# Performance work log

Hardware: AMD Instinct MI355X
Metric: run time of the kernel (lower is better)

The kernel has to match this reference:

```python
import jax, jax.numpy as jnp
import numpy as np

N_NODES = 100000
N_EDGES = 640000
EMB = 128
BATCH = 16384
N_REL = 2
HIDDEN = [128, 64, 32]
LN_EPS = 1e-5
NORM_EPS = 1e-12


def setup_inputs() -> dict:
    key = jax.random.key(0)
    ks = jax.random.split(key, 24)
    inp = {}
    inp["user_indices"] = jax.random.randint(ks[0], (BATCH,), 0, N_NODES)
    inp["item_indices"] = jax.random.randint(ks[1], (BATCH,), 0, N_NODES)
    inp["edge_index"] = jax.random.randint(ks[2], (2, N_EDGES), 0, N_NODES)
    inp["edge_type"] = jax.random.randint(ks[3], (N_EDGES,), 0, N_REL)
    inp["edge_weight"] = jax.random.uniform(ks[4], (N_EDGES,), dtype=jnp.float32)
    # parameters
    s = 1.0 / np.sqrt(EMB)
    inp["embedding"] = jax.random.normal(ks[5], (N_NODES, EMB), jnp.float32) * 0.02
    inp["w1_rel"] = jax.random.normal(ks[6], (N_REL, EMB, EMB), jnp.float32) * s
    inp["w1_root"] = jax.random.normal(ks[7], (EMB, EMB), jnp.float32) * s
    inp["b1"] = jnp.zeros((EMB,), jnp.float32)
    inp["ln_g"] = jnp.ones((EMB,), jnp.float32)
    inp["ln_b"] = jnp.zeros((EMB,), jnp.float32)
    inp["w2_rel"] = jax.random.normal(ks[8], (N_REL, EMB, EMB), jnp.float32) * s
    inp["w2_root"] = jax.random.normal(ks[9], (EMB, EMB), jnp.float32) * s
    inp["b2"] = jnp.zeros((EMB,), jnp.float32)
    dims = [2 * EMB] + HIDDEN
    for i in range(len(HIDDEN)):
        inp[f"mlp_w{i}"] = jax.random.normal(ks[10 + i], (dims[i], dims[i + 1]), jnp.float32) / np.sqrt(dims[i])
        inp[f"mlp_b{i}"] = jnp.zeros((dims[i + 1],), jnp.float32)
    d_out = HIDDEN[-1] + EMB
    inp["out_w"] = jax.random.normal(ks[20], (d_out, 1), jnp.float32) / np.sqrt(d_out)
    inp["out_b"] = jnp.zeros((1,), jnp.float32)
    return inp


def rgcn_layer(x, edge_index, edge_type, edge_weight, w_rel, w_root, bias):
    # x: [N, D]; edge_index: [2, E]; per-relation linear on gathered source feats,
    # weighted scatter-add into destination nodes, plus root transform + bias.
    src, dst = edge_index[0], edge_index[1]
    x_j = x[src]  # [E, D] gather
    msg = jnp.zeros((x_j.shape[0], w_rel.shape[2]), x.dtype)
    for r in range(w_rel.shape[0]):  # small fixed relation count
        msg = msg + jnp.where((edge_type == r)[:, None], x_j @ w_rel[r], 0.0)
    msg = msg * edge_weight[:, None]
    agg = jax.ops.segment_sum(msg, dst, num_segments=x.shape[0])
    return agg + x @ w_root + bias


def layer_norm(x, g, b):
    mu = jnp.mean(x, axis=-1, keepdims=True)
    var = jnp.mean(jnp.square(x - mu), axis=-1, keepdims=True)
    return (x - mu) * jax.lax.rsqrt(var + LN_EPS) * g + b


def l2_normalize(x):
    n = jnp.sqrt(jnp.sum(jnp.square(x), axis=-1, keepdims=True))
    return x / jnp.maximum(n, NORM_EPS)


def reference(user_indices, item_indices, edge_index, edge_type, edge_weight,
              embedding, w1_rel, w1_root, b1, ln_g, ln_b, w2_rel, w2_root, b2,
              mlp_w0, mlp_b0, mlp_w1, mlp_b1, mlp_w2, mlp_b2, out_w, out_b):
    x = embedding  # embedding(arange(N)) == full table
    x = rgcn_layer(x, edge_index, edge_type, edge_weight, w1_rel, w1_root, b1)
    x = jax.nn.relu(x)
    # dropout is identity in eval mode
    x = layer_norm(x, ln_g, ln_b)
    x = rgcn_layer(x, edge_index, edge_type, edge_weight, w2_rel, w2_root, b2)

    u = x[user_indices]  # [B, D]
    v = x[item_indices]
    gmf = l2_normalize(u) * l2_normalize(v)  # [B, D]
    h = jnp.concatenate([u, v], axis=-1)  # [B, 2D]
    for w, b in ((mlp_w0, mlp_b0), (mlp_w1, mlp_b1), (mlp_w2, mlp_b2)):
        h = jax.nn.relu(h @ w + b)
    final = jnp.concatenate([gmf, h], axis=-1)  # [B, D + 32]
    score = jax.nn.sigmoid(final @ out_w + out_b)
    return jnp.squeeze(score, axis=-1)
```

## Files before the change

kernel.cpp:

```cpp
#include <hip/hip_runtime.h>
#include <cstddef>
#include <cstdint>

#define N_NODES 100000
#define N_EDGES 640000
#define EMBD    128
#define NBATCH  16384
#define CHUNK   1024
#define NCHUNK  ((N_NODES + CHUNK - 1) / CHUNK)

typedef short bf16x8 __attribute__((ext_vector_type(8)));
typedef float f32x4  __attribute__((ext_vector_type(4)));

__device__ __forceinline__ unsigned pack_split(float x) {
    unsigned u  = __float_as_uint(x);
    unsigned hi = (u + 0x7fffu + ((u >> 16) & 1u)) & 0xffff0000u;
    float    lo = x - __uint_as_float(hi);
    unsigned ul = __float_as_uint(lo);
    unsigned lw = ((ul + 0x7fffu + ((ul >> 16) & 1u)) >> 16) & 0xffffu;
    return hi | lw;
}
__device__ __forceinline__ float unpack_split(unsigned u) {
    return __uint_as_float(u & 0xffff0000u) + __uint_as_float(u << 16);
}

__global__ __launch_bounds__(256) void pack_hist(
    const float* __restrict__ emb, unsigned* __restrict__ xslot,
    const int* __restrict__ ei, int* __restrict__ cursor, int n, int E)
{
    const int i = blockIdx.x * 256 + threadIdx.x;
    if (i < n) xslot[i] = pack_split(emb[i]);
    if (i < E) atomicAdd(&cursor[ei[E + i]], 1);
}

__global__ __launch_bounds__(256) void scan_local(
    int* __restrict__ cursor, int* __restrict__ bsum, int n)
{
    __shared__ int part[256];
    const int t    = threadIdx.x;
    const int base = blockIdx.x * CHUNK + t * 4;
    int v[4];
    int s = 0;
#pragma unroll
    for (int i = 0; i < 4; ++i) {
        const int idx = base + i;
        v[i] = (idx < n) ? cursor[idx] : 0;
        s += v[i];
    }
    part[t] = s;
    __syncthreads();
    for (int off = 1; off < 256; off <<= 1) {
        const int add = (t >= off) ? part[t - off] : 0;
        __syncthreads();
        part[t] += add;
        __syncthreads();
    }
    if (t == 255) bsum[blockIdx.x] = part[255];
    int run = (t == 0) ? 0 : part[t - 1];
#pragma unroll
    for (int i = 0; i < 4; ++i) {
        const int idx = base + i;
        if (idx < n) { cursor[idx] = run; run += v[i]; }
    }
}

__global__ __launch_bounds__(128) void scan_bsum(int* __restrict__ bsum)
{
    __shared__ int part[128];
    const int t = threadIdx.x;
    const int v = (t < NCHUNK) ? bsum[t] : 0;
    part[t] = v;
    __syncthreads();
    for (int off = 1; off < 128; off <<= 1) {
        const int add = (t >= off) ? part[t - off] : 0;
        __syncthreads();
        part[t] += add;
        __syncthreads();
    }
    if (t < NCHUNK) bsum[t] = part[t] - v;
}

__global__ __launch_bounds__(256) void scan_add(
    int* __restrict__ cursor, const int* __restrict__ bsum, int n)
{
    const int off  = bsum[blockIdx.x];
    const int base = blockIdx.x * CHUNK + threadIdx.x * 4;
#pragma unroll
    for (int i = 0; i < 4; ++i) {
        const int idx = base + i;
        if (idx < n) cursor[idx] += off;
    }
}

__global__ __launch_bounds__(256) void bucket_kernel(
    const int* __restrict__ ei, const int* __restrict__ et,
    const float* __restrict__ ew, int* __restrict__ cursor,
    int2* __restrict__ srec, int E)
{
    const int e = blockIdx.x * 256 + threadIdx.x;
    if (e >= E) return;
    const int src = ei[e];
    const int dst = ei[E + e];
    const int r   = et[e];
    const int pos = atomicAdd(&cursor[dst], 1);
    srec[pos] = make_int2(src | (r << 17), __float_as_int(ew[e]));
}

__global__ __launch_bounds__(256) void accum_csr(
    const unsigned* __restrict__ xp, const int2* __restrict__ srec,
    const int* __restrict__ cursor, unsigned* __restrict__ Ap, int N)
{
    const int wid  = blockIdx.x * 4 + (threadIdx.x >> 6);
    const int lane = threadIdx.x & 63;
    const int s = (wid == 0) ? 0 : cursor[wid - 1];
    const int e = cursor[wid];

    float ax = 0.f, ay = 0.f, bx = 0.f, by = 0.f;
    int i = s;
    for (; i + 3 < e; i += 4) {
        const int2 r0 = srec[i];
        const int2 r1 = srec[i + 1];
        const int2 r2 = srec[i + 2];
        const int2 r3 = srec[i + 3];
        const uint2 g0 = ((const uint2*)(xp + (size_t)(r0.x & 0x1FFFF) * EMBD))[lane];
        const uint2 g1 = ((const uint2*)(xp + (size_t)(r1.x & 0x1FFFF) * EMBD))[lane];
        const uint2 g2 = ((const uint2*)(xp + (size_t)(r2.x & 0x1FFFF) * EMBD))[lane];
        const uint2 g3 = ((const uint2*)(xp + (size_t)(r3.x & 0x1FFFF) * EMBD))[lane];
        const float w0 = __int_as_float(r0.y);
        const float w1 = __int_as_float(r1.y);
        const float w2 = __int_as_float(r2.y);
        const float w3 = __int_as_float(r3.y);
        {
            const float vx = unpack_split(g0.x), vy = unpack_split(g0.y);
            if (r0.x & (1 << 17)) { bx += vx * w0; by += vy * w0; }
            else                  { ax += vx * w0; ay += vy * w0; }
        }
        {
            const float vx = unpack_split(g1.x), vy = unpack_split(g1.y);
            if (r1.x & (1 << 17)) { bx += vx * w1; by += vy * w1; }
            else                  { ax += vx * w1; ay += vy * w1; }
        }
        {
            const float vx = unpack_split(g2.x), vy = unpack_split(g2.y);
            if (r2.x & (1 << 17)) { bx += vx * w2; by += vy * w2; }
            else                  { ax += vx * w2; ay += vy * w2; }
        }
        {
            const float vx = unpack_split(g3.x), vy = unpack_split(g3.y);
            if (r3.x & (1 << 17)) { bx += vx * w3; by += vy * w3; }
            else                  { ax += vx * w3; ay += vy * w3; }
        }
    }
    for (; i < e; ++i) {
        const int2 r0 = srec[i];
        const uint2 g0 = ((const uint2*)(xp + (size_t)(r0.x & 0x1FFFF) * EMBD))[lane];
        const float w0 = __int_as_float(r0.y);
        const float vx = unpack_split(g0.x), vy = unpack_split(g0.y);
        if (r0.x & (1 << 17)) { bx += vx * w0; by += vy * w0; }
        else                  { ax += vx * w0; ay += vy * w0; }
    }
    ((uint2*)(Ap + (size_t)wid * EMBD))[lane]       = make_uint2(pack_split(ax), pack_split(ay));
    ((uint2*)(Ap + ((size_t)N + wid) * EMBD))[lane] = make_uint2(pack_split(bx), pack_split(by));
}

__global__ __launch_bounds__(256) void gemm_mfma(
    const unsigned* __restrict__ S0, const unsigned* __restrict__ S1,
    const unsigned* __restrict__ S2,
    const float* __restrict__ wrel, const float* __restrict__ wroot,
    const float* __restrict__ bias, const float* __restrict__ lng,
    const float* __restrict__ lnb, void* __restrict__ outv,
    int M, int do_ln)
{
    __shared__ unsigned short AsH[128 * 40], AsL[128 * 40];
    __shared__ unsigned short BsH[128 * 40], BsL[128 * 40];
    __shared__ float lnbuf[2][128][2];

    const int t    = threadIdx.x;
    const int wave = t >> 6;
    const int lane = t & 63;
    const int q    = lane >> 4;
    const int n    = lane & 15;
    const int wrow = wave & 1;
    const int wcol = wave >> 1;
    const int m0   = blockIdx.x * 128;

    const int arow  = t >> 1;
    const int ahalf = t & 1;
    const int bcol  = t & 127;
    const int bkh   = t >> 7;

    f32x4 acc[4][4];
#pragma unroll
    for (int rt = 0; rt < 4; ++rt)
#pragma unroll
        for (int ct = 0; ct < 4; ++ct)
            acc[rt][ct] = (f32x4){0.f, 0.f, 0.f, 0.f};

    uint4 au0, au1, au2, au3;
    auto loadA = [&](int kc) {
        const unsigned* Sp = (kc < 4) ? S0 : (kc < 8) ? S1 : S2;
        const int rg = m0 + arow;
        if (rg < M) {
            const unsigned* p = Sp + (size_t)rg * EMBD + (kc & 3) * 32 + ahalf * 16;
            au0 = *(const uint4*)(p);
            au1 = *(const uint4*)(p + 4);
            au2 = *(const uint4*)(p + 8);
            au3 = *(const uint4*)(p + 12);
        } else {
            au0 = au1 = au2 = au3 = make_uint4(0u, 0u, 0u, 0u);
        }
    };

    loadA(0);

    for (int kc = 0; kc < 12; ++kc) {
        __syncthreads();

        {
            const unsigned uu[16] = {au0.x, au0.y, au0.z, au0.w,
                                     au1.x, au1.y, au1.z, au1.w,
                                     au2.x, au2.y, au2.z, au2.w,
                                     au3.x, au3.y, au3.z, au3.w};
            unsigned dh[8], dl[8];
#pragma unroll
            for (int i = 0; i < 8; ++i) {
                const unsigned e0 = uu[2 * i], e1 = uu[2 * i + 1];
                dh[i] = (e1 & 0xffff0000u) | (e0 >> 16);
                dl[i] = (e1 << 16) | (e0 & 0xffffu);
            }
            uint4* pH = (uint4*)(AsH + arow * 40 + ahalf * 16);
            uint4* pL = (uint4*)(AsL + arow * 40 + ahalf * 16);
            pH[0] = make_uint4(dh[0], dh[1], dh[2], dh[3]);
            pH[1] = make_uint4(dh[4], dh[5], dh[6], dh[7]);
            pL[0] = make_uint4(dl[0], dl[1], dl[2], dl[3]);
            pL[1] = make_uint4(dl[4], dl[5], dl[6], dl[7]);
        }

        if (kc < 11) loadA(kc + 1);

        {
            const float* Wsrc = (kc < 8) ? (wrel + (size_t)kc * 32 * EMBD)
                                         : (wroot + (size_t)(kc - 8) * 32 * EMBD);
            unsigned pk[16];
#pragma unroll
            for (int j = 0; j < 16; ++j)
                pk[j] = pack_split(Wsrc[(size_t)(bkh * 16 + j) * EMBD + bcol]);
            unsigned dh[8], dl[8];
#pragma unroll
            for (int i = 0; i < 8; ++i) {
                const unsigned e0 = pk[2 * i], e1 = pk[2 * i + 1];
                dh[i] = (e1 & 0xffff0000u) | (e0 >> 16);
                dl[i] = (e1 << 16) | (e0 & 0xffffu);
            }
            uint4* pH = (uint4*)(BsH + bcol * 40 + bkh * 16);
            uint4* pL = (uint4*)(BsL + bcol * 40 + bkh * 16);
            pH[0] = make_uint4(dh[0], dh[1], dh[2], dh[3]);
            pH[1] = make_uint4(dh[4], dh[5], dh[6], dh[7]);
            pL[0] = make_uint4(dl[0], dl[1], dl[2], dl[3]);
            pL[1] = make_uint4(dl[4], dl[5], dl[6], dl[7]);
        }
        __syncthreads();

        bf16x8 ah[4], al[4];
#pragma unroll
        for (int rt = 0; rt < 4; ++rt) {
            const int r = wrow * 64 + rt * 16 + n;
            ah[rt] = *(const bf16x8*)&AsH[r * 40 + q * 8];
            al[rt] = *(const bf16x8*)&AsL[r * 40 + q * 8];
        }
#pragma unroll
        for (int ct = 0; ct < 4; ++ct) {
            const int c = wcol * 64 + ct * 16 + n;
            const bf16x8 bh = *(const bf16x8*)&BsH[c * 40 + q * 8];
            const bf16x8 bl = *(const bf16x8*)&BsL[c * 40 + q * 8];
#pragma unroll
            for (int rt = 0; rt < 4; ++rt) {
                acc[rt][ct] = __builtin_amdgcn_mfma_f32_16x16x32_bf16(ah[rt], bh, acc[rt][ct], 0, 0, 0);
                acc[rt][ct] = __builtin_amdgcn_mfma_f32_16x16x32_bf16(ah[rt], bl, acc[rt][ct], 0, 0, 0);
                acc[rt][ct] = __builtin_amdgcn_mfma_f32_16x16x32_bf16(al[rt], bh, acc[rt][ct], 0, 0, 0);
            }
        }
    }

    float bb[4], gg[4], tb[4];
#pragma unroll
    for (int ct = 0; ct < 4; ++ct) {
        const int c = wcol * 64 + ct * 16 + n;
        bb[ct] = bias[c];
        gg[ct] = do_ln ? lng[c] : 0.f;
        tb[ct] = do_ln ? lnb[c] : 0.f;
    }

    if (do_ln) {
#pragma unroll
        for (int rt = 0; rt < 4; ++rt)
#pragma unroll
            for (int r = 0; r < 4; ++r) {
                float s = 0.f, sq = 0.f;
#pragma unroll
                for (int ct = 0; ct < 4; ++ct) {
                    float v = acc[rt][ct][r] + bb[ct];
                    v = fmaxf(v, 0.f);
                    acc[rt][ct][r] = v;
                    s += v; sq += v * v;
                }
#pragma unroll
                for (int off = 1; off < 16; off <<= 1) {
                    s  += __shfl_xor(s,  off, 64);
                    sq += __shfl_xor(sq, off, 64);
                }
                if (n == 0) {
                    const int row = wrow * 64 + rt * 16 + q * 4 + r;
                    lnbuf[wcol][row][0] = s;
                    lnbuf[wcol][row][1] = sq;
                }
            }
        __syncthreads();
        unsigned* outp = (unsigned*)outv;
#pragma unroll
        for (int rt = 0; rt < 4; ++rt)
#pragma unroll
            for (int r = 0; r < 4; ++r) {
                const int row = wrow * 64 + rt * 16 + q * 4 + r;
                const int rg  = m0 + row;
                const float s    = lnbuf[0][row][0] + lnbuf[1][row][0];
                const float sq   = lnbuf[0][row][1] + lnbuf[1][row][1];
                const float mu   = s * (1.0f / 128.0f);
                const float var  = sq * (1.0f / 128.0f) - mu * mu;
                const float rstd = rsqrtf(var + 1e-5f);
                if (rg < M) {
#pragma unroll
                    for (int ct = 0; ct < 4; ++ct) {
                        const int c = wcol * 64 + ct * 16 + n;
                        const float v = (acc[rt][ct][r] - mu) * rstd * gg[ct] + tb[ct];
                        outp[(size_t)rg * EMBD + c] = pack_split(v);
                    }
                }
            }
    } else {
        float* outp = (float*)outv;
#pragma unroll
        for (int rt = 0; rt < 4; ++rt)
#pragma unroll
            for (int r = 0; r < 4; ++r) {
                const int rg = m0 + wrow * 64 + rt * 16 + q * 4 + r;
                if (rg < M) {
#pragma unroll
                    for (int ct = 0; ct < 4; ++ct) {
                        const int c = wcol * 64 + ct * 16 + n;
                        outp[(size_t)rg * EMBD + c] = acc[rt][ct][r] + bb[ct];
                    }
                }
            }
    }
}

__global__ __launch_bounds__(256) void head_kernel(
    const float* __restrict__ x2, const int* __restrict__ ui, const int* __restrict__ vi,
    const float* __restrict__ mw0, const float* __restrict__ mb0,
    const float* __restrict__ mw1, const float* __restrict__ mb1,
    const float* __restrict__ mw2, const float* __restrict__ mb2,
    const float* __restrict__ ow, const float* __restrict__ ob,
    float* __restrict__ out, int B)
{
    __shared__ float h0[16][256];
    __shared__ float h1[16][128];
    __shared__ float h2[16][64];
    __shared__ float h3[16][32];
    __shared__ float ps_u[16][16], ps_v[16][16];
    __shared__ float inv_nunv[16];
    __shared__ float pg[16][16], ph[16][16];

    const int t   = threadIdx.x;
    const int bb0 = blockIdx.x * 16;

    for (int r = 0; r < 16; ++r) {
        const int b   = bb0 + r;
        const int idx = (t < 128) ? ui[b] : vi[b];
        const int c   = t & 127;
        h0[r][t] = x2[(size_t)idx * EMBD + c];
    }
    __syncthreads();

    {
        const int row = t >> 4, sub = t & 15;
        float su = 0.f, sv = 0.f;
#pragma unroll
        for (int k = 0; k < 8; ++k) {
            const float a = h0[row][sub + 16 * k];       su += a * a;
            const float b = h0[row][128 + sub + 16 * k]; sv += b * b;
        }
        ps_u[row][sub] = su; ps_v[row][sub] = sv;
    }
    __syncthreads();
    if (t < 16) {
        float su = 0.f, sv = 0.f;
#pragma unroll
        for (int k = 0; k < 16; ++k) { su += ps_u[t][k]; sv += ps_v[t][k]; }
        const float nu = fmaxf(sqrtf(su), 1e-12f);
        const float nv = fmaxf(sqrtf(sv), 1e-12f);
        inv_nunv[t] = 1.0f / (nu * nv);
    }
    __syncthreads();

    {
        const int c = t & 127, rr = t >> 7;
        float acc[8];
#pragma unroll
        for (int j = 0; j < 8; ++j) acc[j] = 0.f;
        for (int i = 0; i < 256; i += 4) {
            const float w0 = mw0[(i + 0) * 128 + c];
            const float w1 = mw0[(i + 1) * 128 + c];
            const float w2 = mw0[(i + 2) * 128 + c];
            const float w3 = mw0[(i + 3) * 128 + c];
#pragma unroll
            for (int j = 0; j < 8; ++j) {
                const float4 a = *(const float4*)&h0[rr * 8 + j][i];
                acc[j] += a.x * w0 + a.y * w1 + a.z * w2 + a.w * w3;
            }
        }
        const float bv = mb0[c];
#pragma unroll
        for (int j = 0; j < 8; ++j) h1[rr * 8 + j][c] = fmaxf(acc[j] + bv, 0.f);
    }
    __syncthreads();

    {
        const int c = t & 63, g = t >> 6;
        float acc[4] = {0.f, 0.f, 0.f, 0.f};
        for (int i = 0; i < 128; i += 4) {
            const float w0 = mw1[(i + 0) * 64 + c];
            const float w1 = mw1[(i + 1) * 64 + c];
            const float w2 = mw1[(i + 2) * 64 + c];
            const float w3 = mw1[(i + 3) * 64 + c];
#pragma unroll
            for (int j = 0; j < 4; ++j) {
                const float4 a = *(const float4*)&h1[g * 4 + j][i];
                acc[j] += a.x * w0 + a.y * w1 + a.z * w2 + a.w * w3;
            }
        }
        const float bv = mb1[c];
#pragma unroll
        for (int j = 0; j < 4; ++j) h2[g * 4 + j][c] = fmaxf(acc[j] + bv, 0.f);
    }
    __syncthreads();

    {
        const int c = t & 31, g = t >> 5;
        float acc[2] = {0.f, 0.f};
        for (int i = 0; i < 64; i += 4) {
            const float w0 = mw2[(i + 0) * 32 + c];
            const float w1 = mw2[(i + 1) * 32 + c];
            const float w2 = mw2[(i + 2) * 32 + c];
            const float w3 = mw2[(i + 3) * 32 + c];
#pragma unroll
            for (int j = 0; j < 2; ++j) {
                const float4 a = *(const float4*)&h2[g * 2 + j][i];
                acc[j] += a.x * w0 + a.y * w1 + a.z * w2 + a.w * w3;
            }
        }
        const float bv = mb2[c];
#pragma unroll
        for (int j = 0; j < 2; ++j) h3[g * 2 + j][c] = fmaxf(acc[j] + bv, 0.f);
    }
    __syncthreads();

    {
        const int row = t >> 4, sub = t & 15;
        float pgv = 0.f;
#pragma unroll
        for (int k = 0; k < 8; ++k) {
            const int c = sub + 16 * k;
            pgv += h0[row][c] * h0[row][128 + c] * ow[c];
        }
        const float phv = h3[row][sub]      * ow[128 + sub]
                        + h3[row][sub + 16] * ow[144 + sub];
        pg[row][sub] = pgv; ph[row][sub] = phv;
    }
    __syncthreads();
    if (t < 16) {
        float sg = 0.f, sh = 0.f;
#pragma unroll
        for (int k = 0; k < 16; ++k) { sg += pg[t][k]; sh += ph[t][k]; }
        const float z = sg * inv_nunv[t] + sh + ob[0];
        out[bb0 + t] = 1.0f / (1.0f + expf(-z));
    }
}

extern "C" void kernel_launch(void* const* d_in, const int* in_sizes, int n_in,
                              void* d_out, int out_size, void* d_ws, size_t ws_size,
                              hipStream_t stream)
{
    const int*   ui      = (const int*)d_in[0];
    const int*   vi      = (const int*)d_in[1];
    const int*   ei      = (const int*)d_in[2];
    const int*   et      = (const int*)d_in[3];
    const float* ew      = (const float*)d_in[4];
    const float* emb     = (const float*)d_in[5];
    const float* w1_rel  = (const float*)d_in[6];
    const float* w1_root = (const float*)d_in[7];
    const float* b1      = (const float*)d_in[8];
    const float* ln_g    = (const float*)d_in[9];
    const float* ln_b    = (const float*)d_in[10];
    const float* w2_rel  = (const float*)d_in[11];
    const float* w2_root = (const float*)d_in[12];
    const float* b2      = (const float*)d_in[13];
    const float* mw0     = (const float*)d_in[14];
    const float* mb0     = (const float*)d_in[15];
    const float* mw1     = (const float*)d_in[16];
    const float* mb1     = (const float*)d_in[17];
    const float* mw2     = (const float*)d_in[18];
    const float* mb2     = (const float*)d_in[19];
    const float* ow      = (const float*)d_in[20];
    const float* ob      = (const float*)d_in[21];
    float* out = (float*)d_out;

    const int N = N_NODES, E = N_EDGES, B = NBATCH;

    unsigned* Ap    = (unsigned*)d_ws;
    unsigned* xslot = Ap + (size_t)2 * N * EMBD;
    int2*     srec   = (int2*)(xslot + (size_t)N * EMBD);
    int*      cursor = (int*)(srec + E);
    int*      bsum   = cursor + N;

    float* x2 = (float*)Ap;

    hipMemsetAsync(cursor, 0, N * sizeof(int), stream);
    pack_hist<<<(N * EMBD + 255) / 256, 256, 0, stream>>>(emb, xslot, ei, cursor, N * EMBD, E);

    scan_local<<<NCHUNK, 256, 0, stream>>>(cursor, bsum, N);
    scan_bsum<<<1, 128, 0, stream>>>(bsum);
    scan_add<<<NCHUNK, 256, 0, stream>>>(cursor, bsum, N);
    bucket_kernel<<<(E + 255) / 256, 256, 0, stream>>>(ei, et, ew, cursor, srec, E);

    const int ggrid = (N + 127) / 128;

    accum_csr<<<N / 4, 256, 0, stream>>>(xslot, srec, cursor, Ap, N);
    gemm_mfma<<<ggrid, 256, 0, stream>>>(
        Ap, Ap + (size_t)N * EMBD, xslot,
        w1_rel, w1_root, b1, ln_g, ln_b, (void*)xslot, N, 1);

    accum_csr<<<N / 4, 256, 0, stream>>>(xslot, srec, cursor, Ap, N);
    gemm_mfma<<<ggrid, 256, 0, stream>>>(
        Ap, Ap + (size_t)N * EMBD, xslot,
        w2_rel, w2_root, b2, nullptr, nullptr, (void*)x2, N, 0);

    head_kernel<<<B / 16, 256, 0, stream>>>(
        x2, ui, vi, mw0, mb0, mw1, mb1, mw2, mb2, ow, ob, out, B);
}
```

Measured before the change: 499.7 us.

## Split node features into bf16 hi/lo planes and gather only the hi plane

Features are stored as separate bf16 high and low planes instead of interleaved hi/lo words. The edge aggregation now gathers only the high plane and writes its result as plain bf16. This halves the bytes moved by the memory-bound gather and halves the aggregate writes. The GEMM drops the low-part MFMA for the aggregated operand and skips the repacking shuffle. The separate block-sum scan kernel is folded into scan_add, which removes one launch. The cost is lower precision in the message aggregation, since the low-order correction bits of source features and aggregates are discarded.

New measurement: 597.0 us. 19.5% more time.

```diff
diff --git a/kernel.cpp b/kernel.cpp
--- a/kernel.cpp
+++ b/kernel.cpp
@@ -20,16 +20,25 @@
     unsigned lw = ((ul + 0x7fffu + ((ul >> 16) & 1u)) >> 16) & 0xffffu;
     return hi | lw;
 }
-__device__ __forceinline__ float unpack_split(unsigned u) {
-    return __uint_as_float(u & 0xffff0000u) + __uint_as_float(u << 16);
+__device__ __forceinline__ unsigned short f2bf(float x) {
+    unsigned u = __float_as_uint(x);
+    return (unsigned short)((u + 0x7fffu + ((u >> 16) & 1u)) >> 16);
+}
+__device__ __forceinline__ float bf2f(unsigned short h) {
+    return __uint_as_float((unsigned)h << 16);
 }
 
 __global__ __launch_bounds__(256) void pack_hist(
-    const float* __restrict__ emb, unsigned* __restrict__ xslot,
+    const float* __restrict__ emb,
+    unsigned short* __restrict__ xhi, unsigned short* __restrict__ xlo,
     const int* __restrict__ ei, int* __restrict__ cursor, int n, int E)
 {
     const int i = blockIdx.x * 256 + threadIdx.x;
-    if (i < n) xslot[i] = pack_split(emb[i]);
+    if (i < n) {
+        const unsigned p = pack_split(emb[i]);
+        xhi[i] = (unsigned short)(p >> 16);
+        xlo[i] = (unsigned short)(p & 0xffffu);
+    }
     if (i < E) atomicAdd(&cursor[ei[E + i]], 1);
 }
 
@@ -64,31 +73,24 @@
     }
 }
 
-__global__ __launch_bounds__(128) void scan_bsum(int* __restrict__ bsum)
-{
-    __shared__ int part[128];
-    const int t = threadIdx.x;
-    const int v = (t < NCHUNK) ? bsum[t] : 0;
-    part[t] = v;
-    __syncthreads();
-    for (int off = 1; off < 128; off <<= 1) {
-        const int add = (t >= off) ? part[t - off] : 0;
-        __syncthreads();
-        part[t] += add;
-        __syncthreads();
-    }
-    if (t < NCHUNK) bsum[t] = part[t] - v;
-}
-
 __global__ __launch_bounds__(256) void scan_add(
     int* __restrict__ cursor, const int* __restrict__ bsum, int n)
 {
-    const int off  = bsum[blockIdx.x];
-    const int base = blockIdx.x * CHUNK + threadIdx.x * 4;
+    __shared__ int red[256];
+    const int t = threadIdx.x;
+    const int b = blockIdx.x;
+    red[t] = (t < b && t < NCHUNK) ? bsum[t] : 0;
+    __syncthreads();
+    for (int off = 128; off > 0; off >>= 1) {
+        if (t < off) red[t] += red[t + off];
+        __syncthreads();
+    }
+    const int off_ = red[0];
+    const int base = b * CHUNK + t * 4;
 #pragma unroll
     for (int i = 0; i < 4; ++i) {
         const int idx = base + i;
-        if (idx < n) cursor[idx] += off;
+        if (idx < n) cursor[idx] += off_;
     }
 }
 
@@ -107,8 +109,8 @@
 }
 
 __global__ __launch_bounds__(256) void accum_csr(
-    const unsigned* __restrict__ xp, const int2* __restrict__ srec,
-    const int* __restrict__ cursor, unsigned* __restrict__ Ap, int N)
+    const unsigned short* __restrict__ xhi, const int2* __restrict__ srec,
+    const int* __restrict__ cursor, unsigned short* __restrict__ Ahi, int N)
 {
     const int wid  = blockIdx.x * 4 + (threadIdx.x >> 6);
     const int lane = threadIdx.x & 63;
@@ -122,54 +124,63 @@
         const int2 r1 = srec[i + 1];
         const int2 r2 = srec[i + 2];
         const int2 r3 = srec[i + 3];
-        const uint2 g0 = ((const uint2*)(xp + (size_t)(r0.x & 0x1FFFF) * EMBD))[lane];
-        const uint2 g1 = ((const uint2*)(xp + (size_t)(r1.x & 0x1FFFF) * EMBD))[lane];
-        const uint2 g2 = ((const uint2*)(xp + (size_t)(r2.x & 0x1FFFF) * EMBD))[lane];
-        const uint2 g3 = ((const uint2*)(xp + (size_t)(r3.x & 0x1FFFF) * EMBD))[lane];
+        const unsigned g0 = ((const unsigned*)(xhi + (size_t)(r0.x & 0x1FFFF) * EMBD))[lane];
+        const unsigned g1 = ((const unsigned*)(xhi + (size_t)(r1.x & 0x1FFFF) * EMBD))[lane];
+        const unsigned g2 = ((const unsigned*)(xhi + (size_t)(r2.x & 0x1FFFF) * EMBD))[lane];
+        const unsigned g3 = ((const unsigned*)(xhi + (size_t)(r3.x & 0x1FFFF) * EMBD))[lane];
         const float w0 = __int_as_float(r0.y);
         const float w1 = __int_as_float(r1.y);
         const float w2 = __int_as_float(r2.y);
         const float w3 = __int_as_float(r3.y);
         {
-            const float vx = unpack_split(g0.x), vy = unpack_split(g0.y);
+            const float vx = bf2f((unsigned short)(g0 & 0xffffu));
+            const float vy = bf2f((unsigned short)(g0 >> 16));
             if (r0.x & (1 << 17)) { bx += vx * w0; by += vy * w0; }
             else                  { ax += vx * w0; ay += vy * w0; }
         }
         {
-            const float vx = unpack_split(g1.x), vy = unpack_split(g1.y);
+            const float vx = bf2f((unsigned short)(g1 & 0xffffu));
+            const float vy = bf2f((unsigned short)(g1 >> 16));
             if (r1.x & (1 << 17)) { bx += vx * w1; by += vy * w1; }
             else                  { ax += vx * w1; ay += vy * w1; }
         }
         {
-            const float vx = unpack_split(g2.x), vy = unpack_split(g2.y);
+            const float vx = bf2f((unsigned short)(g2 & 0xffffu));
+            const float vy = bf2f((unsigned short)(g2 >> 16));
             if (r2.x & (1 << 17)) { bx += vx * w2; by += vy * w2; }
             else                  { ax += vx * w2; ay += vy * w2; }
         }
         {
-            const float vx = unpack_split(g3.x), vy = unpack_split(g3.y);
+            const float vx = bf2f((unsigned short)(g3 & 0xffffu));
+            const float vy = bf2f((unsigned short)(g3 >> 16));
             if (r3.x & (1 << 17)) { bx += vx * w3; by += vy * w3; }
             else                  { ax += vx * w3; ay += vy * w3; }
         }
     }
     for (; i < e; ++i) {
         const int2 r0 = srec[i];
-        const uint2 g0 = ((const uint2*)(xp + (size_t)(r0.x & 0x1FFFF) * EMBD))[lane];
+        const unsigned g0 = ((const unsigned*)(xhi + (size_t)(r0.x & 0x1FFFF) * EMBD))[lane];
         const float w0 = __int_as_float(r0.y);
-        const float vx = unpack_split(g0.x), vy = unpack_split(g0.y);
+        const float vx = bf2f((unsigned short)(g0 & 0xffffu));
+        const float vy = bf2f((unsigned short)(g0 >> 16));
         if (r0.x & (1 << 17)) { bx += vx * w0; by += vy * w0; }
         else                  { ax += vx * w0; ay += vy * w0; }
     }
-    ((uint2*)(Ap + (size_t)wid * EMBD))[lane]       = make_uint2(pack_split(ax), pack_split(ay));
-    ((uint2*)(Ap + ((size_t)N + wid) * EMBD))[lane] = make_uint2(pack_split(bx), pack_split(by));
+    ((unsigned*)(Ahi + (size_t)wid * EMBD))[lane] =
+        (unsigned)f2bf(ax) | ((unsigned)f2bf(ay) << 16);
+    ((unsigned*)(Ahi + ((size_t)N + wid) * EMBD))[lane] =
+        (unsigned)f2bf(bx) | ((unsigned)f2bf(by) << 16);
 }
 
 __global__ __launch_bounds__(256) void gemm_mfma(
-    const unsigned* __restrict__ S0, const unsigned* __restrict__ S1,
-    const unsigned* __restrict__ S2,
+    const unsigned short* __restrict__ Ahi,
+    const unsigned short* __restrict__ xhi, const unsigned short* __restrict__ xlo,
     const float* __restrict__ wrel, const float* __restrict__ wroot,
     const float* __restrict__ bias, const float* __restrict__ lng,
-    const float* __restrict__ lnb, void* __restrict__ outv,
-    int M, int do_ln)
+    const float* __restrict__ lnb,
+    unsigned short* __restrict__ oh, unsigned short* __restrict__ ol,
+    float* __restrict__ of,
+    int M, int N, int do_ln)
 {
     __shared__ unsigned short AsH[128 * 40], AsL[128 * 40];
     __shared__ unsigned short BsH[128 * 40], BsL[128 * 40];
@@ -196,18 +207,24 @@
         for (int ct = 0; ct < 4; ++ct)
             acc[rt][ct] = (f32x4){0.f, 0.f, 0.f, 0.f};
 
-    uint4 au0, au1, au2, au3;
+    uint4 auh0, auh1, aul0, aul1;
     auto loadA = [&](int kc) {
-        const unsigned* Sp = (kc < 4) ? S0 : (kc < 8) ? S1 : S2;
         const int rg = m0 + arow;
         if (rg < M) {
-            const unsigned* p = Sp + (size_t)rg * EMBD + (kc & 3) * 32 + ahalf * 16;
-            au0 = *(const uint4*)(p);
-            au1 = *(const uint4*)(p + 4);
-            au2 = *(const uint4*)(p + 8);
-            au3 = *(const uint4*)(p + 12);
+            if (kc < 8) {
+                const unsigned short* p =
+                    Ahi + ((size_t)((kc >> 2) & 1) * N + rg) * EMBD + (kc & 3) * 32 + ahalf * 16;
+                auh0 = *(const uint4*)(p);
+                auh1 = *(const uint4*)(p + 8);
+            } else {
+                const size_t o = (size_t)rg * EMBD + (kc - 8) * 32 + ahalf * 16;
+                auh0 = *(const uint4*)(xhi + o);
+                auh1 = *(const uint4*)(xhi + o + 8);
+                aul0 = *(const uint4*)(xlo + o);
+                aul1 = *(const uint4*)(xlo + o + 8);
+            }
         } else {
-            au0 = au1 = au2 = au3 = make_uint4(0u, 0u, 0u, 0u);
+            auh0 = auh1 = aul0 = aul1 = make_uint4(0u, 0u, 0u, 0u);
         }
     };
 
@@ -217,23 +234,12 @@
         __syncthreads();
 
         {
-            const unsigned uu[16] = {au0.x, au0.y, au0.z, au0.w,
-                                     au1.x, au1.y, au1.z, au1.w,
-                                     au2.x, au2.y, au2.z, au2.w,
-                                     au3.x, au3.y, au3.z, au3.w};
-            unsigned dh[8], dl[8];
-#pragma unroll
-            for (int i = 0; i < 8; ++i) {
-                const unsigned e0 = uu[2 * i], e1 = uu[2 * i + 1];
-                dh[i] = (e1 & 0xffff0000u) | (e0 >> 16);
-                dl[i] = (e1 << 16) | (e0 & 0xffffu);
-            }
             uint4* pH = (uint4*)(AsH + arow * 40 + ahalf * 16);
-            uint4* pL = (uint4*)(AsL + arow * 40 + ahalf * 16);
-            pH[0] = make_uint4(dh[0], dh[1], dh[2], dh[3]);
-            pH[1] = make_uint4(dh[4], dh[5], dh[6], dh[7]);
-            pL[0] = make_uint4(dl[0], dl[1], dl[2], dl[3]);
-            pL[1] = make_uint4(dl[4], dl[5], dl[6], dl[7]);
+            pH[0] = auh0; pH[1] = auh1;
+            if (kc >= 8) {
+                uint4* pL = (uint4*)(AsL + arow * 40 + ahalf * 16);
+                pL[0] = aul0; pL[1] = aul1;
+            }
         }
 
         if (kc < 11) loadA(kc + 1);
@@ -261,23 +267,42 @@
         }
         __syncthreads();
 
-        bf16x8 ah[4], al[4];
+        bf16x8 ah[4];
 #pragma unroll
         for (int rt = 0; rt < 4; ++rt) {
             const int r = wrow * 64 + rt * 16 + n;
             ah[rt] = *(const bf16x8*)&AsH[r * 40 + q * 8];
-            al[rt] = *(const bf16x8*)&AsL[r * 40 + q * 8];
-        }
-#pragma unroll
-        for (int ct = 0; ct < 4; ++ct) {
-            const int c = wcol * 64 + ct * 16 + n;
-            const bf16x8 bh = *(const bf16x8*)&BsH[c * 40 + q * 8];
-            const bf16x8 bl = *(const bf16x8*)&BsL[c * 40 + q * 8];
+        }
+        if (kc < 8) {
+#pragma unroll
+            for (int ct = 0; ct < 4; ++ct) {
+                const int c = wcol * 64 + ct * 16 + n;
+                const bf16x8 bh = *(const bf16x8*)&BsH[c * 40 + q * 8];
+                const bf16x8 bl = *(const bf16x8*)&BsL[c * 40 + q * 8];
+#pragma unroll
+                for (int rt = 0; rt < 4; ++rt) {
+                    acc[rt][ct] = __builtin_amdgcn_mfma_f32_16x16x32_bf16(ah[rt], bh, acc[rt][ct], 0, 0, 0);
+                    acc[rt][ct] = __builtin_amdgcn_mfma_f32_16x16x32_bf16(ah[rt], bl, acc[rt][ct], 0, 0, 0);
+                }
+            }
+        } else {
+            bf16x8 al[4];
 #pragma unroll
             for (int rt = 0; rt < 4; ++rt) {
-                acc[rt][ct] = __builtin_amdgcn_mfma_f32_16x16x32_bf16(ah[rt], bh, acc[rt][ct], 0, 0, 0);
-                acc[rt][ct] = __builtin_amdgcn_mfma_f32_16x16x32_bf16(ah[rt], bl, acc[rt][ct], 0, 0, 0);
-                acc[rt][ct] = __builtin_amdgcn_mfma_f32_16x16x32_bf16(al[rt], bh, acc[rt][ct], 0, 0, 0);
+                const int r = wrow * 64 + rt * 16 + n;
+                al[rt] = *(const bf16x8*)&AsL[r * 40 + q * 8];
+            }
+#pragma unroll
+            for (int ct = 0; ct < 4; ++ct) {
+                const int c = wcol * 64 + ct * 16 + n;
+                const bf16x8 bh = *(const bf16x8*)&BsH[c * 40 + q * 8];
+                const bf16x8 bl = *(const bf16x8*)&BsL[c * 40 + q * 8];
+#pragma unroll
+                for (int rt = 0; rt < 4; ++rt) {
+                    acc[rt][ct] = __builtin_amdgcn_mfma_f32_16x16x32_bf16(ah[rt], bh, acc[rt][ct], 0, 0, 0);
+                    acc[rt][ct] = __builtin_amdgcn_mfma_f32_16x16x32_bf16(ah[rt], bl, acc[rt][ct], 0, 0, 0);
+                    acc[rt][ct] = __builtin_amdgcn_mfma_f32_16x16x32_bf16(al[rt], bh, acc[rt][ct], 0, 0, 0);
+                }
             }
         }
     }
@@ -316,7 +341,6 @@
                 }
             }
         __syncthreads();
-        unsigned* outp = (unsigned*)outv;
 #pragma unroll
         for (int rt = 0; rt < 4; ++rt)
 #pragma unroll
@@ -333,12 +357,13 @@
                     for (int ct = 0; ct < 4; ++ct) {
                         const int c = wcol * 64 + ct * 16 + n;
                         const float v = (acc[rt][ct][r] - mu) * rstd * gg[ct] + tb[ct];
-                        outp[(size_t)rg * EMBD + c] = pack_split(v);
+                        const unsigned p = pack_split(v);
+                        oh[(size_t)rg * EMBD + c] = (unsigned short)(p >> 16);
+                        ol[(size_t)rg * EMBD + c] = (unsigned short)(p & 0xffffu);
                     }
                 }
             }
     } else {
-        float* outp = (float*)outv;
 #pragma unroll
         for (int rt = 0; rt < 4; ++rt)
 #pragma unroll
@@ -348,7 +373,7 @@
 #pragma unroll
                     for (int ct = 0; ct < 4; ++ct) {
                         const int c = wcol * 64 + ct * 16 + n;
-                        outp[(size_t)rg * EMBD + c] = acc[rt][ct][r] + bb[ct];
+                        of[(size_t)rg * EMBD + c] = acc[rt][ct][r] + bb[ct];
                     }
                 }
             }
@@ -517,33 +542,33 @@
 
     const int N = N_NODES, E = N_EDGES, B = NBATCH;
 
-    unsigned* Ap    = (unsigned*)d_ws;
-    unsigned* xslot = Ap + (size_t)2 * N * EMBD;
-    int2*     srec   = (int2*)(xslot + (size_t)N * EMBD);
-    int*      cursor = (int*)(srec + E);
-    int*      bsum   = cursor + N;
-
-    float* x2 = (float*)Ap;
+    unsigned short* Ahi = (unsigned short*)d_ws;
+    unsigned short* xhi = Ahi + (size_t)2 * N * EMBD;
+    unsigned short* xlo = xhi + (size_t)N * EMBD;
+    float*          x2  = (float*)(xlo + (size_t)N * EMBD);
+    int2*   srec   = (int2*)(x2 + (size_t)N * EMBD);
+    int*    cursor = (int*)(srec + E);
+    int*    bsum   = cursor + N;
 
     hipMemsetAsync(cursor, 0, N * sizeof(int), stream);
-    pack_hist<<<(N * EMBD + 255) / 256, 256, 0, stream>>>(emb, xslot, ei, cursor, N * EMBD, E);
+    pack_hist<<<(N * EMBD + 255) / 256, 256, 0, stream>>>(
+        emb, xhi, xlo, ei, cursor, N * EMBD, E);
 
     scan_local<<<NCHUNK, 256, 0, stream>>>(cursor, bsum, N);
-    scan_bsum<<<1, 128, 0, stream>>>(bsum);
     scan_add<<<NCHUNK, 256, 0, stream>>>(cursor, bsum, N);
     bucket_kernel<<<(E + 255) / 256, 256, 0, stream>>>(ei, et, ew, cursor, srec, E);
 
     const int ggrid = (N + 127) / 128;
 
-    accum_csr<<<N / 4, 256, 0, stream>>>(xslot, srec, cursor, Ap, N);
+    accum_csr<<<N / 4, 256, 0, stream>>>(xhi, srec, cursor, Ahi, N);
     gemm_mfma<<<ggrid, 256, 0, stream>>>(
-        Ap, Ap + (size_t)N * EMBD, xslot,
-        w1_rel, w1_root, b1, ln_g, ln_b, (void*)xslot, N, 1);
-
-    accum_csr<<<N / 4, 256, 0, stream>>>(xslot, srec, cursor, Ap, N);
+        Ahi, xhi, xlo, w1_rel, w1_root, b1, ln_g, ln_b,
+        xhi, xlo, nullptr, N, N, 1);
+
+    accum_csr<<<N / 4, 256, 0, stream>>>(xhi, srec, cursor, Ahi, N);
     gemm_mfma<<<ggrid, 256, 0, stream>>>(
-        Ap, Ap + (size_t)N * EMBD, xslot,
-        w2_rel, w2_root, b2, nullptr, nullptr, (void*)x2, N, 0);
+        Ahi, xhi, xlo, w2_rel, w2_root, b2, nullptr, nullptr,
+        nullptr, nullptr, x2, N, N, 0);
 
     head_kernel<<<B / 16, 256, 0, stream>>>(
         x2, ui, vi, mw0, mb0, mw1, mb1, mw2, mb2, ow, ob, out, B);
```

## Gather bf16-only feature copy in edge aggregation and fold block-sum scan

Applied to the files above, without the earlier changes.

Writes a second, bf16-high-half-only copy of node features (in pack_hist and the LN gemm epilogue) and has the CSR aggregation gather that copy, halving gather bytes per edge. It also removes the single-block scan_bsum kernel by having each scan_add block reduce its prefix of block sums itself, and vectorises pack_hist to two floats per thread. The new path drops the low bf16 correction term, which loses precision in messages, and it needs extra workspace, falling back to the old path when the workspace is too small.

Result: faster. 482.6 us (-3.4%).

```diff
diff --git a/kernel.cpp b/kernel.cpp
--- a/kernel.cpp
+++ b/kernel.cpp
@@ -23,14 +23,24 @@
 __device__ __forceinline__ float unpack_split(unsigned u) {
     return __uint_as_float(u & 0xffff0000u) + __uint_as_float(u << 16);
 }
+__device__ __forceinline__ float bf2f(unsigned short h) {
+    return __uint_as_float((unsigned)h << 16);
+}
 
 __global__ __launch_bounds__(256) void pack_hist(
-    const float* __restrict__ emb, unsigned* __restrict__ xslot,
-    const int* __restrict__ ei, int* __restrict__ cursor, int n, int E)
-{
-    const int i = blockIdx.x * 256 + threadIdx.x;
-    if (i < n) xslot[i] = pack_split(emb[i]);
-    if (i < E) atomicAdd(&cursor[ei[E + i]], 1);
+    const float* __restrict__ emb, unsigned* __restrict__ xp,
+    unsigned short* __restrict__ xh,
+    const int* __restrict__ ei, int* __restrict__ cursor, int n2, int E)
+{
+    const int j = blockIdx.x * 256 + threadIdx.x;
+    if (j < n2) {
+        const float2 v = ((const float2*)emb)[j];
+        const unsigned p0 = pack_split(v.x);
+        const unsigned p1 = pack_split(v.y);
+        ((uint2*)xp)[j] = make_uint2(p0, p1);
+        if (xh) ((unsigned*)xh)[j] = (p0 >> 16) | (p1 & 0xffff0000u);
+    }
+    if (j < E) atomicAdd(&cursor[ei[E + j]], 1);
 }
 
 __global__ __launch_bounds__(256) void scan_local(
@@ -64,31 +74,24 @@
     }
 }
 
-__global__ __launch_bounds__(128) void scan_bsum(int* __restrict__ bsum)
-{
-    __shared__ int part[128];
-    const int t = threadIdx.x;
-    const int v = (t < NCHUNK) ? bsum[t] : 0;
-    part[t] = v;
-    __syncthreads();
-    for (int off = 1; off < 128; off <<= 1) {
-        const int add = (t >= off) ? part[t - off] : 0;
-        __syncthreads();
-        part[t] += add;
-        __syncthreads();
-    }
-    if (t < NCHUNK) bsum[t] = part[t] - v;
-}
-
 __global__ __launch_bounds__(256) void scan_add(
     int* __restrict__ cursor, const int* __restrict__ bsum, int n)
 {
-    const int off  = bsum[blockIdx.x];
-    const int base = blockIdx.x * CHUNK + threadIdx.x * 4;
+    __shared__ int red[256];
+    const int t = threadIdx.x;
+    const int b = blockIdx.x;
+    red[t] = (t < b && t < NCHUNK) ? bsum[t] : 0;
+    __syncthreads();
+    for (int off = 128; off > 0; off >>= 1) {
+        if (t < off) red[t] += red[t + off];
+        __syncthreads();
+    }
+    const int off_ = red[0];
+    const int base = b * CHUNK + t * 4;
 #pragma unroll
     for (int i = 0; i < 4; ++i) {
         const int idx = base + i;
-        if (idx < n) cursor[idx] += off;
+        if (idx < n) cursor[idx] += off_;
     }
 }
 
@@ -106,9 +109,11 @@
     srec[pos] = make_int2(src | (r << 17), __float_as_int(ew[e]));
 }
 
+template <bool HI>
 __global__ __launch_bounds__(256) void accum_csr(
-    const unsigned* __restrict__ xp, const int2* __restrict__ srec,
-    const int* __restrict__ cursor, unsigned* __restrict__ Ap, int N)
+    const unsigned* __restrict__ xp, const unsigned short* __restrict__ xh,
+    const int2* __restrict__ srec, const int* __restrict__ cursor,
+    unsigned* __restrict__ Ap, int N)
 {
     const int wid  = blockIdx.x * 4 + (threadIdx.x >> 6);
     const int lane = threadIdx.x & 63;
@@ -116,48 +121,50 @@
     const int e = cursor[wid];
 
     float ax = 0.f, ay = 0.f, bx = 0.f, by = 0.f;
+
+    auto fetch = [&](int src, float& vx, float& vy) {
+        if (HI) {
+            const unsigned g = ((const unsigned*)(xh + (size_t)src * EMBD))[lane];
+            vx = bf2f((unsigned short)(g & 0xffffu));
+            vy = bf2f((unsigned short)(g >> 16));
+        } else {
+            const uint2 g = ((const uint2*)(xp + (size_t)src * EMBD))[lane];
+            vx = unpack_split(g.x);
+            vy = unpack_split(g.y);
+        }
+    };
+
     int i = s;
     for (; i + 3 < e; i += 4) {
         const int2 r0 = srec[i];
         const int2 r1 = srec[i + 1];
         const int2 r2 = srec[i + 2];
         const int2 r3 = srec[i + 3];
-        const uint2 g0 = ((const uint2*)(xp + (size_t)(r0.x & 0x1FFFF) * EMBD))[lane];
-        const uint2 g1 = ((const uint2*)(xp + (size_t)(r1.x & 0x1FFFF) * EMBD))[lane];
-        const uint2 g2 = ((const uint2*)(xp + (size_t)(r2.x & 0x1FFFF) * EMBD))[lane];
-        const uint2 g3 = ((const uint2*)(xp + (size_t)(r3.x & 0x1FFFF) * EMBD))[lane];
+        float x0, y0, x1, y1, x2v, y2v, x3, y3;
+        fetch(r0.x & 0x1FFFF, x0, y0);
+        fetch(r1.x & 0x1FFFF, x1, y1);
+        fetch(r2.x & 0x1FFFF, x2v, y2v);
+        fetch(r3.x & 0x1FFFF, x3, y3);
         const float w0 = __int_as_float(r0.y);
         const float w1 = __int_as_float(r1.y);
         const float w2 = __int_as_float(r2.y);
         const float w3 = __int_as_float(r3.y);
-        {
-            const float vx = unpack_split(g0.x), vy = unpack_split(g0.y);
-            if (r0.x & (1 << 17)) { bx += vx * w0; by += vy * w0; }
-            else                  { ax += vx * w0; ay += vy * w0; }
-        }
-        {
-            const float vx = unpack_split(g1.x), vy = unpack_split(g1.y);
-            if (r1.x & (1 << 17)) { bx += vx * w1; by += vy * w1; }
-            else                  { ax += vx * w1; ay += vy * w1; }
-        }
-        {
-            const float vx = unpack_split(g2.x), vy = unpack_split(g2.y);
-            if (r2.x & (1 << 17)) { bx += vx * w2; by += vy * w2; }
-            else                  { ax += vx * w2; ay += vy * w2; }
-        }
-        {
-            const float vx = unpack_split(g3.x), vy = unpack_split(g3.y);
-            if (r3.x & (1 << 17)) { bx += vx * w3; by += vy * w3; }
-            else                  { ax += vx * w3; ay += vy * w3; }
-        }
+        if (r0.x & (1 << 17)) { bx += x0 * w0;  by += y0 * w0; }
+        else                  { ax += x0 * w0;  ay += y0 * w0; }
+        if (r1.x & (1 << 17)) { bx += x1 * w1;  by += y1 * w1; }
+        else                  { ax += x1 * w1;  ay += y1 * w1; }
+        if (r2.x & (1 << 17)) { bx += x2v * w2; by += y2v * w2; }
+        else                  { ax += x2v * w2; ay += y2v * w2; }
+        if (r3.x & (1 << 17)) { bx += x3 * w3;  by += y3 * w3; }
+        else                  { ax += x3 * w3;  ay += y3 * w3; }
     }
     for (; i < e; ++i) {
         const int2 r0 = srec[i];
-        const uint2 g0 = ((const uint2*)(xp + (size_t)(r0.x & 0x1FFFF) * EMBD))[lane];
+        float x0, y0;
+        fetch(r0.x & 0x1FFFF, x0, y0);
         const float w0 = __int_as_float(r0.y);
-        const float vx = unpack_split(g0.x), vy = unpack_split(g0.y);
-        if (r0.x & (1 << 17)) { bx += vx * w0; by += vy * w0; }
-        else                  { ax += vx * w0; ay += vy * w0; }
+        if (r0.x & (1 << 17)) { bx += x0 * w0; by += y0 * w0; }
+        else                  { ax += x0 * w0; ay += y0 * w0; }
     }
     ((uint2*)(Ap + (size_t)wid * EMBD))[lane]       = make_uint2(pack_split(ax), pack_split(ay));
     ((uint2*)(Ap + ((size_t)N + wid) * EMBD))[lane] = make_uint2(pack_split(bx), pack_split(by));
@@ -169,6 +176,7 @@
     const float* __restrict__ wrel, const float* __restrict__ wroot,
     const float* __restrict__ bias, const float* __restrict__ lng,
     const float* __restrict__ lnb, void* __restrict__ outv,
+    unsigned short* __restrict__ ohi,
     int M, int do_ln)
 {
     __shared__ unsigned short AsH[128 * 40], AsL[128 * 40];
@@ -333,7 +341,9 @@
                     for (int ct = 0; ct < 4; ++ct) {
                         const int c = wcol * 64 + ct * 16 + n;
                         const float v = (acc[rt][ct][r] - mu) * rstd * gg[ct] + tb[ct];
-                        outp[(size_t)rg * EMBD + c] = pack_split(v);
+                        const unsigned p = pack_split(v);
+                        outp[(size_t)rg * EMBD + c] = p;
+                        if (ohi) ohi[(size_t)rg * EMBD + c] = (unsigned short)(p >> 16);
                     }
                 }
             }
@@ -517,33 +527,40 @@
 
     const int N = N_NODES, E = N_EDGES, B = NBATCH;
 
-    unsigned* Ap    = (unsigned*)d_ws;
-    unsigned* xslot = Ap + (size_t)2 * N * EMBD;
-    int2*     srec   = (int2*)(xslot + (size_t)N * EMBD);
-    int*      cursor = (int*)(srec + E);
-    int*      bsum   = cursor + N;
+    unsigned* Ap = (unsigned*)d_ws;
+    unsigned* xp = Ap + (size_t)2 * N * EMBD;
+    int2*   srec   = (int2*)(xp + (size_t)N * EMBD);
+    int*    cursor = (int*)(srec + E);
+    int*    bsum   = cursor + N;
+    unsigned short* xhi = (unsigned short*)(bsum + NCHUNK);
+
+    const size_t need_hi = (size_t)((char*)(xhi + (size_t)N * EMBD) - (char*)d_ws);
+    const bool have_hi = (ws_size >= need_hi);
+    unsigned short* xh = have_hi ? xhi : nullptr;
 
     float* x2 = (float*)Ap;
 
     hipMemsetAsync(cursor, 0, N * sizeof(int), stream);
-    pack_hist<<<(N * EMBD + 255) / 256, 256, 0, stream>>>(emb, xslot, ei, cursor, N * EMBD, E);
+    pack_hist<<<(N * EMBD / 2 + 255) / 256, 256, 0, stream>>>(
+        emb, xp, xh, ei, cursor, N * EMBD / 2, E);
 
     scan_local<<<NCHUNK, 256, 0, stream>>>(cursor, bsum, N);
-    scan_bsum<<<1, 128, 0, stream>>>(bsum);
     scan_add<<<NCHUNK, 256, 0, stream>>>(cursor, bsum, N);
     bucket_kernel<<<(E + 255) / 256, 256, 0, stream>>>(ei, et, ew, cursor, srec, E);
 
     const int ggrid = (N + 127) / 128;
 
-    accum_csr<<<N / 4, 256, 0, stream>>>(xslot, srec, cursor, Ap, N);
+    if (have_hi) accum_csr<true ><<<N / 4, 256, 0, stream>>>(xp, xh, srec, cursor, Ap, N);
+    else         accum_csr<false><<<N / 4, 256, 0, stream>>>(xp, xh, srec, cursor, Ap, N);
     gemm_mfma<<<ggrid, 256, 0, stream>>>(
-        Ap, Ap + (size_t)N * EMBD, xslot,
-        w1_rel, w1_root, b1, ln_g, ln_b, (void*)xslot, N, 1);
-
-    accum_csr<<<N / 4, 256, 0, stream>>>(xslot, srec, cursor, Ap, N);
+        Ap, Ap + (size_t)N * EMBD, xp,
+        w1_rel, w1_root, b1, ln_g, ln_b, (void*)xp, xh, N, 1);
+
+    if (have_hi) accum_csr<true ><<<N / 4, 256, 0, stream>>>(xp, xh, srec, cursor, Ap, N);
+    else         accum_csr<false><<<N / 4, 256, 0, stream>>>(xp, xh, srec, cursor, Ap, N);
     gemm_mfma<<<ggrid, 256, 0, stream>>>(
-        Ap, Ap + (size_t)N * EMBD, xslot,
-        w2_rel, w2_root, b2, nullptr, nullptr, (void*)x2, N, 0);
+        Ap, Ap + (size_t)N * EMBD, xp,
+        w2_rel, w2_root, b2, nullptr, nullptr, (void*)x2, nullptr, N, 0);
 
     head_kernel<<<B / 16, 256, 0, stream>>>(
         x2, ui, vi, mw0, mb0, mw1, mb1, mw2, mb2, ow, ob, out, B);
```
